# Kernel optimization log

Measured on AMD Instinct MI355X. Metric: run time of the kernel, lower is better.

The kernel has to match this reference:

```python
import jax, jax.numpy as jnp
import numpy as np

N, L, E, H = 8, 1024, 512, 4


def setup_inputs() -> dict:
    key = jax.random.key(0)
    ks = jax.random.split(key, 10)
    s = 1.0 / np.sqrt(E)
    return {
        "modalA": jax.random.normal(ks[0], (N, L, E), dtype=jnp.float32),
        "modalB": jax.random.normal(ks[1], (N, L, E), dtype=jnp.float32),
        "WqA": jax.random.normal(ks[2], (E, E), dtype=jnp.float32) * s,
        "bqA": jax.random.normal(ks[3], (E,), dtype=jnp.float32) * s,
        "WkA": jax.random.normal(ks[4], (E, E), dtype=jnp.float32) * s,
        "bkA": jax.random.normal(ks[5], (E,), dtype=jnp.float32) * s,
        "WqB": jax.random.normal(ks[6], (E, E), dtype=jnp.float32) * s,
        "bqB": jax.random.normal(ks[7], (E,), dtype=jnp.float32) * s,
        "WkB": jax.random.normal(ks[8], (E, E), dtype=jnp.float32) * s,
        "bkB": jax.random.normal(ks[9], (E,), dtype=jnp.float32) * s,
    }


def reference(modalA, modalB, WqA, bqA, WkA, bkA, WqB, bqB, WkB, bkB):
    # torch Linear: y = x @ W.T + b
    qA = modalA @ WqA.T + bqA  # [N, L, E]
    kA = modalA @ WkA.T + bkA
    qB = modalB @ WqB.T + bqB
    kB = modalB @ WkB.T + bkB

    # mean over heads of per-head dot products == full-dim dot / num_heads
    # (algebraically identical to einsum('nqhd,nkhd->nhqk').mean(1))
    inv_scale = 1.0 / (H * np.sqrt(E).astype(np.float32))

    def attn(q, k):
        scores = jnp.einsum('nqd,nkd->nqk', q, k) * inv_scale  # [N, L, L]
        return jax.nn.softmax(scores, axis=-1)

    weighted_A = attn(qA, kA)
    weighted_B = attn(qB, kB)
    weighted_AB = attn(qA, kB)
    weighted_BA = attn(qB, kA)

    cat_lower = jnp.concatenate([weighted_A, weighted_AB], axis=-1)  # [N, L, 2L]
    cat_upper = jnp.concatenate([weighted_B, weighted_BA], axis=-1)  # [N, L, 2L]
    cat = jnp.concatenate([cat_lower, cat_upper], axis=1)            # [N, 2L, 2L]
    return jnp.mean(cat, axis=0)                                     # [2L, 2L]
```

## Files before the change

kernel.cpp:

```cpp
#include <hip/hip_runtime.h>
#include <hip/hip_bf16.h>

typedef __bf16 bf16;
typedef bf16 bf16x8 __attribute__((ext_vector_type(8)));
typedef _Float16 f16;
typedef f16 f16x8 __attribute__((ext_vector_type(8)));
typedef float f32x4 __attribute__((ext_vector_type(4)));

constexpr int LL = 1024;
constexpr int EE = 512;
constexpr int NBATCH = 8;

__device__ __forceinline__ f32x4 mfma16(bf16x8 a, bf16x8 b, f32x4 c) {
    return __builtin_amdgcn_mfma_f32_16x16x32_bf16(a, b, c, 0, 0, 0);
}

#define GLOAD_LDS16(g, l)                                                     \
    __builtin_amdgcn_global_load_lds(                                         \
        (const __attribute__((address_space(1))) void*)(g),                   \
        (__attribute__((address_space(3))) void*)(l), 16, 0, 0)

constexpr int WAIT_VM4_LG0 = 0x074;
constexpr int WAIT_VM0_LG0 = 0x070;

template <int IMM>
__device__ __forceinline__ void pipe_barrier() {
    __asm__ volatile("" ::: "memory");
    __builtin_amdgcn_s_waitcnt(IMM);
    __builtin_amdgcn_sched_barrier(0);
    __builtin_amdgcn_s_barrier();
    __builtin_amdgcn_sched_barrier(0);
    __asm__ volatile("" ::: "memory");
}

struct CvtParams {
    const float* src[4];
    bf16* dst[4];
    int n8[4];
};

__global__ __launch_bounds__(256) void cvt_kernel(CvtParams p) {
    const int y = blockIdx.y;
    const float* __restrict__ src = p.src[y];
    bf16* __restrict__ dst = p.dst[y];
    const int n8 = p.n8[y];
    for (int i = blockIdx.x * 256 + threadIdx.x; i < n8; i += gridDim.x * 256) {
        float4 a = *(const float4*)(src + (size_t)i * 8);
        float4 b = *(const float4*)(src + (size_t)i * 8 + 4);
        bf16x8 o;
        o[0] = (bf16)a.x; o[1] = (bf16)a.y; o[2] = (bf16)a.z; o[3] = (bf16)a.w;
        o[4] = (bf16)b.x; o[5] = (bf16)b.y; o[6] = (bf16)b.z; o[7] = (bf16)b.w;
        *(bf16x8*)(dst + (size_t)i * 8) = o;
    }
}

struct ProjParams {
    const float* x[4];
    const bf16* w[4];
    const float* b[4];
};

__global__ __launch_bounds__(256, 2) void proj_kernel(ProjParams p, bf16* __restrict__ outbase) {
    const int f = blockIdx.x;
    const int xcd = f & 7;
    const int u = f >> 3;
    const int mz = xcd >> 2;
    const int by = (xcd & 3) * 16 + (u & 15);
    const int zq = (u >> 4) & 1;
    const int bxp = u >> 5;
    const int z = mz * 2 + zq;

    const float* __restrict__ X = p.x[z];
    const bf16* __restrict__ W = p.w[z];
    const float* __restrict__ Bv = p.b[z];
    bf16* __restrict__ O = outbase + (size_t)z * (NBATCH * LL) * EE;

    __shared__ union {
        struct {
            alignas(16) float Af[2][128][32];
            alignas(16) bf16  Bs[2][256][32];
        } st;
        alignas(16) bf16 ep[64][264];
    } sm;

    const int t = threadIdx.x;
    const int lane = t & 63, wid = t >> 6;
    const int wm = wid & 1, wn = wid >> 1;
    const int lr = lane & 15, kg = lane >> 4;

    f32x4 acc[4][8] = {};

    const int ar = t >> 3;
    const int ac = t & 7;
    const int sA = (ar >> 1) & 7;
    const int agc = (ac ^ sA) * 4;
    const float* Xrow0 = X + (size_t)(by * 128 + ar) * EE + agc;

    const int srow = t >> 2;
    const int cgl = t & 3;
    const int gcg = (cgl ^ ((srow >> 1) & 3)) * 8;
    const int scg = (kg ^ ((lr >> 1) & 3)) * 8;
    const bf16* Wrow0 = W + (size_t)(bxp * 256 + srow) * EE + gcg;

    const int cgLo = (2 * kg) ^ ((lr >> 1) & 7);
    const int cgHi = cgLo ^ 1;

    auto stage = [&](int k, int b) {
        const int k0 = k * 32;
#pragma unroll
        for (int i = 0; i < 4; ++i)
            GLOAD_LDS16(Xrow0 + (size_t)(32 * i) * EE + k0, &sm.st.Af[b][32 * i + ar][ac * 4]);
#pragma unroll
        for (int i = 0; i < 4; ++i)
            GLOAD_LDS16(Wrow0 + (size_t)(64 * i) * EE + k0, &sm.st.Bs[b][srow + 64 * i][cgl * 8]);
    };
    auto compute = [&](int b) {
        bf16x8 af[4], bfr[8];
#pragma unroll
        for (int im = 0; im < 4; ++im) {
            const int row = wm * 64 + im * 16 + lr;
            f32x4 lo = *(const f32x4*)&sm.st.Af[b][row][cgLo * 4];
            f32x4 hi = *(const f32x4*)&sm.st.Af[b][row][cgHi * 4];
#pragma unroll
            for (int e = 0; e < 4; ++e) {
                af[im][e] = (bf16)lo[e];
                af[im][4 + e] = (bf16)hi[e];
            }
        }
#pragma unroll
        for (int in = 0; in < 8; ++in)
            bfr[in] = *(const bf16x8*)&sm.st.Bs[b][wn * 128 + in * 16 + lr][scg];
#pragma unroll
        for (int im = 0; im < 4; ++im)
#pragma unroll
            for (int in = 0; in < 8; ++in)
                acc[im][in] = mfma16(af[im], bfr[in], acc[im][in]);
    };

    stage(0, 0);
#pragma unroll
    for (int k = 0; k < 16; ++k) {
        pipe_barrier<WAIT_VM0_LG0>();
        if (k < 15) stage(k + 1, (k + 1) & 1);
        compute(k & 1);
    }
    __syncthreads();

#pragma unroll
    for (int pph = 0; pph < 2; ++pph) {
        if (wm == pph) {
#pragma unroll
            for (int im = 0; im < 4; ++im) {
                const int row = im * 16 + kg * 4;
#pragma unroll
                for (int in = 0; in < 8; ++in) {
                    const int col = wn * 128 + in * 16 + lr;
                    const float bias = Bv[bxp * 256 + col];
#pragma unroll
                    for (int r = 0; r < 4; ++r)
                        sm.ep[row + r][col] = (bf16)(acc[im][in][r] + bias);
                }
            }
        }
        __syncthreads();
#pragma unroll
        for (int i = 0; i < 8; ++i) {
            const int c = i * 256 + t;
            const int row = c >> 5, colg = (c & 31) * 8;
            *(uint4*)(O + (size_t)(by * 128 + pph * 64 + row) * EE + bxp * 256 + colg) =
                *(const uint4*)&sm.ep[row][colg];
        }
        __syncthreads();
    }
}

struct ScoresParams {
    const bf16* q[4];
    const bf16* k[4];
    f16* s[4];
};

__global__ __launch_bounds__(512, 2) void scores_kernel(ScoresParams p) {
    const int f = blockIdx.x;
    const int xcd = f & 7;
    const int j = f >> 3;
    const int z = (xcd << 2) + (j >> 4);
    const int map = z >> 3, n = z & 7;
    const int tile = j & 15;
    const int bx = tile & 3, by = tile >> 2;

    const bf16* __restrict__ Qb = p.q[map] + (size_t)n * LL * EE;
    const bf16* __restrict__ Kb = p.k[map] + (size_t)n * LL * EE;
    f16* __restrict__ Sb = p.s[map] + (size_t)n * LL * LL;

    __shared__ union {
        struct { alignas(16) bf16 A[3][256][32]; alignas(16) bf16 B[3][256][32]; } st;
        alignas(16) f16 ep[128][264];
    } sm;

    const int t = threadIdx.x;
    const int lane = t & 63, wid = t >> 6;
    const int wm = wid & 1, wn = wid >> 1;
    const int lr = lane & 15, kg = lane >> 4;

    f32x4 acc[8][4] = {};

    const int srow = t >> 2;
    const int cgl = t & 3;
    const int gcg = (cgl ^ ((srow >> 1) & 3)) * 8;
    const int scg = (kg ^ ((lr >> 1) & 3)) * 8;

    const bf16* Qrow0 = Qb + (size_t)(by * 256 + srow) * EE + gcg;
    const bf16* Krow0 = Kb + (size_t)(bx * 256 + srow) * EE + gcg;

    auto stage = [&](int k, int b) {
        const int k0 = k * 32;
#pragma unroll
        for (int i = 0; i < 2; ++i)
            GLOAD_LDS16(Qrow0 + (size_t)(128 * i) * EE + k0, &sm.st.A[b][srow + 128 * i][cgl * 8]);
#pragma unroll
        for (int i = 0; i < 2; ++i)
            GLOAD_LDS16(Krow0 + (size_t)(128 * i) * EE + k0, &sm.st.B[b][srow + 128 * i][cgl * 8]);
    };
    auto compute = [&](int b) {
        bf16x8 af[8], bfr[4];
#pragma unroll
        for (int im = 0; im < 8; ++im)
            af[im] = *(const bf16x8*)&sm.st.A[b][wm * 128 + im * 16 + lr][scg];
#pragma unroll
        for (int in = 0; in < 4; ++in)
            bfr[in] = *(const bf16x8*)&sm.st.B[b][wn * 64 + in * 16 + lr][scg];
#pragma unroll
        for (int im = 0; im < 8; ++im)
#pragma unroll
            for (int in = 0; in < 4; ++in)
                acc[im][in] = mfma16(af[im], bfr[in], acc[im][in]);
    };

    stage(0, 0);
    stage(1, 1);
#pragma unroll
    for (int k = 0; k < 16; ++k) {
        if (k < 15) pipe_barrier<WAIT_VM4_LG0>();
        else        pipe_barrier<WAIT_VM0_LG0>();
        if (k < 14) stage(k + 2, (k + 2) % 3);
        compute(k % 3);
    }
    __syncthreads();

    const float inv_scale = 0.011048543456039806f;
#pragma unroll
    for (int pph = 0; pph < 2; ++pph) {
        if (wm == pph) {
#pragma unroll
            for (int im = 0; im < 8; ++im) {
                const int row = im * 16 + kg * 4;
#pragma unroll
                for (int in = 0; in < 4; ++in) {
                    const int col = wn * 64 + in * 16 + lr;
#pragma unroll
                    for (int r = 0; r < 4; ++r)
                        sm.ep[row + r][col] = (f16)(acc[im][in][r] * inv_scale);
                }
            }
        }
        __syncthreads();
#pragma unroll
        for (int i = 0; i < 8; ++i) {
            const int c = i * 512 + t;
            const int row = c >> 5, colg = (c & 31) * 8;
            *(uint4*)(Sb + (size_t)(by * 256 + pph * 128 + row) * LL + bx * 256 + colg) =
                *(const uint4*)&sm.ep[row][colg];
        }
        __syncthreads();
    }
}

struct SmParams {
    const f16* s[4];
};

__global__ __launch_bounds__(256) void softmax_mean_kernel(SmParams p, float* __restrict__ out) {
    const int map = blockIdx.y;
    const f16* __restrict__ S = p.s[map];
    const int t = threadIdx.x;
    const int half = t >> 7;
    const int tl = t & 127;
    const int q = blockIdx.x * 2 + half;
    const int lane = t & 63, wid = t >> 6;
    __shared__ float red[NBATCH][4];

    f16x8 v[NBATCH];
#pragma unroll
    for (int n = 0; n < NBATCH; ++n)
        v[n] = *(const f16x8*)(S + ((size_t)n * LL + q) * LL + tl * 8);

    float e[NBATCH][8];
#pragma unroll
    for (int n = 0; n < NBATCH; ++n) {
        float s = 0.f;
#pragma unroll
        for (int j = 0; j < 8; ++j) {
            e[n][j] = __expf((float)v[n][j]);
            s += e[n][j];
        }
#pragma unroll
        for (int off = 32; off; off >>= 1) s += __shfl_xor(s, off);
        if (lane == 0) red[n][wid] = s;
    }
    __syncthreads();

    float acc[8] = {};
#pragma unroll
    for (int n = 0; n < NBATCH; ++n) {
        const float inv = 0.125f / (red[n][half * 2] + red[n][half * 2 + 1]);
#pragma unroll
        for (int j = 0; j < 8; ++j) acc[j] += e[n][j] * inv;
    }

    const int orow = (map >= 2 ? LL : 0) + q;
    const int ocol = (map & 1 ? LL : 0) + tl * 8;
    float* o = out + (size_t)orow * (2 * LL) + ocol;
    *(float4*)(o + 0) = make_float4(acc[0], acc[1], acc[2], acc[3]);
    *(float4*)(o + 4) = make_float4(acc[4], acc[5], acc[6], acc[7]);
}

extern "C" void kernel_launch(void* const* d_in, const int* in_sizes, int n_in,
                              void* d_out, int out_size, void* d_ws, size_t ws_size,
                              hipStream_t stream) {
    const float* modalA = (const float*)d_in[0];
    const float* modalB = (const float*)d_in[1];
    const float* WqA = (const float*)d_in[2];
    const float* bqA = (const float*)d_in[3];
    const float* WkA = (const float*)d_in[4];
    const float* bkA = (const float*)d_in[5];
    const float* WqB = (const float*)d_in[6];
    const float* bqB = (const float*)d_in[7];
    const float* WkB = (const float*)d_in[8];
    const float* bkB = (const float*)d_in[9];
    float* out = (float*)d_out;

    const size_t projN = (size_t)(NBATCH * LL) * EE;
    const size_t mapN = (size_t)NBATCH * LL * LL;
    char* base = (char*)d_ws;
    bf16* qk = (bf16*)base;
    char* region2 = base + 4 * projN * sizeof(bf16);
    bf16* W4 = (bf16*)region2;
    f16* S = (f16*)region2;

    CvtParams cp;
    const float* wsrc[4] = {WqA, WkA, WqB, WkB};
    for (int i = 0; i < 4; ++i) {
        cp.src[i] = wsrc[i];
        cp.dst[i] = W4 + (size_t)i * EE * EE;
        cp.n8[i] = EE * EE / 8;
    }
    cvt_kernel<<<dim3(128, 4), 256, 0, stream>>>(cp);

    ProjParams pp;
    pp.x[0] = modalA; pp.x[1] = modalA; pp.x[2] = modalB; pp.x[3] = modalB;
    for (int i = 0; i < 4; ++i) pp.w[i] = W4 + (size_t)i * EE * EE;
    pp.b[0] = bqA; pp.b[1] = bkA; pp.b[2] = bqB; pp.b[3] = bkB;
    proj_kernel<<<dim3(512), 256, 0, stream>>>(pp, qk);

    const bf16* qA = qk + 0 * projN;
    const bf16* kA = qk + 1 * projN;
    const bf16* qB = qk + 2 * projN;
    const bf16* kB = qk + 3 * projN;

    ScoresParams sp;
    sp.q[0] = qA; sp.q[1] = qA; sp.q[2] = qB; sp.q[3] = qB;
    sp.k[0] = kA; sp.k[1] = kB; sp.k[2] = kB; sp.k[3] = kA;
    for (int m = 0; m < 4; ++m) sp.s[m] = S + (size_t)m * mapN;
    scores_kernel<<<dim3(512), 512, 0, stream>>>(sp);

    SmParams smp;
    for (int m = 0; m < 4; ++m) smp.s[m] = S + (size_t)m * mapN;
    softmax_mean_kernel<<<dim3(512, 4), 256, 0, stream>>>(smp, out);
}
```

Before: 178.9 us.

## Restructure scores GEMM main loop into four-phase ping-pong schedule with K=64 tiles

Replaces the triple-buffered K=32 pipeline in the scores GEMM with a double-buffered K=64 pipeline. Each K tile is split into four MFMA quadrant phases, and global-to-LDS loads for the next tiles are interleaved between them. The phases are separated by barriers, waitcnt and s_setprio to overlap LDS reads, async loads and MFMA work across waves. The wave-to-tile mapping and the LDS swizzle change to match. This adds more barriers per iteration, which could cost more than the overlap gains.

Measured after the change: 179.1 us. About the same (+0.1%).

```diff
diff --git a/kernel.cpp b/kernel.cpp
--- a/kernel.cpp
+++ b/kernel.cpp
@@ -20,13 +20,36 @@
         (const __attribute__((address_space(1))) void*)(g),                   \
         (__attribute__((address_space(3))) void*)(l), 16, 0, 0)
 
+constexpr int WAIT_VM6_LG0 = 0x076;
 constexpr int WAIT_VM4_LG0 = 0x074;
 constexpr int WAIT_VM0_LG0 = 0x070;
+constexpr int WAIT_LG0     = 0xC07F;
 
 template <int IMM>
 __device__ __forceinline__ void pipe_barrier() {
     __asm__ volatile("" ::: "memory");
     __builtin_amdgcn_s_waitcnt(IMM);
+    __builtin_amdgcn_sched_barrier(0);
+    __builtin_amdgcn_s_barrier();
+    __builtin_amdgcn_sched_barrier(0);
+    __asm__ volatile("" ::: "memory");
+}
+
+__device__ __forceinline__ void phase_mid() {
+    __asm__ volatile("" ::: "memory");
+    __builtin_amdgcn_sched_barrier(0);
+    __builtin_amdgcn_s_barrier();
+    __builtin_amdgcn_s_waitcnt(WAIT_LG0);
+    __builtin_amdgcn_sched_barrier(0);
+    __builtin_amdgcn_s_setprio(1);
+    __asm__ volatile("" ::: "memory");
+}
+
+template <int VM>
+__device__ __forceinline__ void phase_end() {
+    __builtin_amdgcn_s_setprio(0);
+    __asm__ volatile("" ::: "memory");
+    if constexpr (VM >= 0) __builtin_amdgcn_s_waitcnt(VM);
     __builtin_amdgcn_sched_barrier(0);
     __builtin_amdgcn_s_barrier();
     __builtin_amdgcn_sched_barrier(0);
@@ -194,57 +217,96 @@
     f16* __restrict__ Sb = p.s[map] + (size_t)n * LL * LL;
 
     __shared__ union {
-        struct { alignas(16) bf16 A[3][256][32]; alignas(16) bf16 B[3][256][32]; } st;
+        struct { alignas(16) bf16 A[2][256][64]; alignas(16) bf16 B[2][256][64]; } st;
         alignas(16) f16 ep[128][264];
     } sm;
 
     const int t = threadIdx.x;
     const int lane = t & 63, wid = t >> 6;
-    const int wm = wid & 1, wn = wid >> 1;
+    const int wm = wid >> 2, wn = wid & 3;
     const int lr = lane & 15, kg = lane >> 4;
+    const int swr = (lr >> 1) & 7;
 
     f32x4 acc[8][4] = {};
 
-    const int srow = t >> 2;
-    const int cgl = t & 3;
-    const int gcg = (cgl ^ ((srow >> 1) & 3)) * 8;
-    const int scg = (kg ^ ((lr >> 1) & 3)) * 8;
-
-    const bf16* Qrow0 = Qb + (size_t)(by * 256 + srow) * EE + gcg;
-    const bf16* Krow0 = Kb + (size_t)(bx * 256 + srow) * EE + gcg;
-
-    auto stage = [&](int k, int b) {
-        const int k0 = k * 32;
+    const int sr = t >> 3;
+    const int sg = t & 7;
+    const int sgsw = sg ^ ((sr >> 1) & 7);
+    const bf16* Qrow = Qb + (size_t)(by * 256 + sr) * EE + sgsw * 8;
+    const bf16* Krow = Kb + (size_t)(bx * 256 + sr) * EE + sgsw * 8;
+
+    auto stageA = [&](int kt, int h) {
+        const int d = kt & 1, k0 = kt * 64;
 #pragma unroll
         for (int i = 0; i < 2; ++i)
-            GLOAD_LDS16(Qrow0 + (size_t)(128 * i) * EE + k0, &sm.st.A[b][srow + 128 * i][cgl * 8]);
+            GLOAD_LDS16(Qrow + (size_t)(h * 128 + i * 64) * EE + k0,
+                        &sm.st.A[d][h * 128 + i * 64 + sr][sg * 8]);
+    };
+    auto stageB = [&](int kt, int h) {
+        const int d = kt & 1, k0 = kt * 64;
 #pragma unroll
         for (int i = 0; i < 2; ++i)
-            GLOAD_LDS16(Krow0 + (size_t)(128 * i) * EE + k0, &sm.st.B[b][srow + 128 * i][cgl * 8]);
-    };
-    auto compute = [&](int b) {
-        bf16x8 af[8], bfr[4];
-#pragma unroll
-        for (int im = 0; im < 8; ++im)
-            af[im] = *(const bf16x8*)&sm.st.A[b][wm * 128 + im * 16 + lr][scg];
-#pragma unroll
-        for (int in = 0; in < 4; ++in)
-            bfr[in] = *(const bf16x8*)&sm.st.B[b][wn * 64 + in * 16 + lr][scg];
-#pragma unroll
-        for (int im = 0; im < 8; ++im)
-#pragma unroll
-            for (int in = 0; in < 4; ++in)
-                acc[im][in] = mfma16(af[im], bfr[in], acc[im][in]);
-    };
-
-    stage(0, 0);
-    stage(1, 1);
-#pragma unroll
-    for (int k = 0; k < 16; ++k) {
-        if (k < 15) pipe_barrier<WAIT_VM4_LG0>();
-        else        pipe_barrier<WAIT_VM0_LG0>();
-        if (k < 14) stage(k + 2, (k + 2) % 3);
-        compute(k % 3);
+            GLOAD_LDS16(Krow + (size_t)(h * 128 + i * 64) * EE + k0,
+                        &sm.st.B[d][h * 128 + i * 64 + sr][sg * 8]);
+    };
+
+    bf16x8 afr0[4][2], afr1[4][2], bfr0[2][2], bfr1[2][2];
+    auto readA = [&](int d, int m, bf16x8 (&dst)[4][2]) {
+#pragma unroll
+        for (int im = 0; im < 4; ++im) {
+            const int row = wm * 128 + m * 64 + im * 16 + lr;
+#pragma unroll
+            for (int s = 0; s < 2; ++s)
+                dst[im][s] = *(const bf16x8*)&sm.st.A[d][row][(((s << 2) + kg) ^ swr) * 8];
+        }
+    };
+    auto readB = [&](int d, int nn, bf16x8 (&dst)[2][2]) {
+#pragma unroll
+        for (int in = 0; in < 2; ++in) {
+            const int row = wn * 64 + nn * 32 + in * 16 + lr;
+#pragma unroll
+            for (int s = 0; s < 2; ++s)
+                dst[in][s] = *(const bf16x8*)&sm.st.B[d][row][(((s << 2) + kg) ^ swr) * 8];
+        }
+    };
+    auto mfmaQ = [&](const bf16x8 (&a)[4][2], const bf16x8 (&b)[2][2], int mb, int nb) {
+#pragma unroll
+        for (int im = 0; im < 4; ++im)
+#pragma unroll
+            for (int in = 0; in < 2; ++in)
+#pragma unroll
+                for (int s = 0; s < 2; ++s)
+                    acc[mb + im][nb + in] = mfma16(a[im][s], b[in][s], acc[mb + im][nb + in]);
+    };
+
+    stageA(0, 0); stageA(0, 1); stageB(0, 0); stageB(0, 1);
+    stageA(1, 0); stageA(1, 1);
+    pipe_barrier<WAIT_VM4_LG0>();
+
+    for (int kt = 0; kt < 8; ++kt) {
+        const int d = kt & 1;
+        readA(d, 0, afr0);
+        readB(d, 0, bfr0);
+        if (kt < 7) stageB(kt + 1, 0);
+        phase_mid();
+        mfmaQ(afr0, bfr0, 0, 0);
+        phase_end<-1>();
+        readA(d, 1, afr1);
+        readB(d, 1, bfr1);
+        if (kt < 7) stageB(kt + 1, 1);
+        phase_mid();
+        mfmaQ(afr0, bfr1, 0, 2);
+        phase_end<-1>();
+        if (kt < 6) stageA(kt + 2, 0);
+        phase_mid();
+        mfmaQ(afr1, bfr1, 4, 2);
+        phase_end<-1>();
+        if (kt < 6) stageA(kt + 2, 1);
+        phase_mid();
+        mfmaQ(afr1, bfr0, 4, 0);
+        if (kt < 6)       phase_end<WAIT_VM4_LG0>();
+        else if (kt == 6) phase_end<WAIT_VM0_LG0>();
+        else              phase_end<-1>();
     }
     __syncthreads();
 
@@ -253,14 +315,14 @@
     for (int pph = 0; pph < 2; ++pph) {
         if (wm == pph) {
 #pragma unroll
-            for (int im = 0; im < 8; ++im) {
-                const int row = im * 16 + kg * 4;
-#pragma unroll
-                for (int in = 0; in < 4; ++in) {
-                    const int col = wn * 64 + in * 16 + lr;
+            for (int mi = 0; mi < 8; ++mi) {
+                const int row = mi * 16 + kg * 4;
+#pragma unroll
+                for (int ni = 0; ni < 4; ++ni) {
+                    const int col = wn * 64 + (ni >> 1) * 32 + (ni & 1) * 16 + lr;
 #pragma unroll
                     for (int r = 0; r < 4; ++r)
-                        sm.ep[row + r][col] = (f16)(acc[im][in][r] * inv_scale);
+                        sm.ep[row + r][col] = (f16)(acc[mi][ni][r] * inv_scale);
                 }
             }
         }
```
